# Optimization experiments

Hardware: AMD Instinct MI355X
Metric: run time of the kernel (lower is better)

The kernel has to match this reference:

```python
import jax, jax.numpy as jnp
import numpy as np

N_NODES = 50000
N_EDGES = 800000
IN_DIM = 128
OUT_DIM = 64
REL_DIM = 32
NEG_SLOPE = 0.01  # torch F.leaky_relu default


def setup_inputs() -> dict:
    key = jax.random.key(0)
    k1, k2, k3, k4, k5, k6 = jax.random.split(key, 6)
    h = jax.random.normal(k1, (N_NODES, IN_DIM), dtype=jnp.float32)
    p = jax.random.normal(k2, (N_EDGES, REL_DIM), dtype=jnp.float32)
    src = jax.random.randint(k3, (N_EDGES,), 0, N_NODES, dtype=jnp.int32)
    dst = jax.random.randint(k4, (N_EDGES,), 0, N_NODES, dtype=jnp.int32)
    # torch Linear weights: [out_features, in_features], xavier-like scale
    W_fc = jax.random.normal(k5, (OUT_DIM, IN_DIM), dtype=jnp.float32) * (2.0 / (IN_DIM + OUT_DIM)) ** 0.5
    W_attn = jax.random.normal(k6, (1, 2 * OUT_DIM + REL_DIM), dtype=jnp.float32) * 0.1
    return {"h": h, "p": p, "src": src, "dst": dst, "W_fc": W_fc, "W_attn": W_attn}


def reference(h, p, src, dst, W_fc, W_attn):
    n = h.shape[0]
    z = h @ W_fc.T                       # [N, out_dim]
    z_src = z[src]                       # [E, out_dim] gather
    z_dst = z[dst]                       # [E, out_dim] gather
    feat = jnp.concatenate([z_src, p, z_dst], axis=1)  # [E, 2*out+rel]
    a = feat @ W_attn.T                  # [E, 1]
    e = jax.nn.leaky_relu(a[:, 0], NEG_SLOPE)          # [E]
    # segment softmax over incoming edges of each dst node
    seg_max = jax.ops.segment_max(e, dst, num_segments=n)  # [N]
    num = jnp.exp(e - seg_max[dst])                        # [E]
    denom = jax.ops.segment_sum(num, dst, num_segments=n)  # [N]
    alpha = num / denom[dst]                               # [E]
    # softmax-weighted message aggregation (scatter-add)
    h_out = jax.ops.segment_sum(alpha[:, None] * z_src, dst, num_segments=n)  # [N, out_dim]
    return h_out
```

## Files before the change

kernel.cpp:

```cpp
#include <hip/hip_runtime.h>
#include <hip/hip_bf16.h>

#define N_NODES 50000
#define N_EDGES 800000
#define IN_DIM 128
#define OUT_DIM 64
#define REL_DIM 32
#define NEG_SLOPE 0.01f
#define NB 391
#define K3_TILE 2048
#define K3_BLOCKS ((N_EDGES + K3_TILE - 1) / K3_TILE)
#define BWIN 2560

typedef __attribute__((ext_vector_type(8))) short bf16x8;
typedef __attribute__((ext_vector_type(4))) float f32x4;

__device__ __forceinline__ short f2bf(float f) {
    unsigned u = __float_as_uint(f);
    u += 0x7FFF + ((u >> 16) & 1);
    return (short)(u >> 16);
}

__global__ __launch_bounds__(256) void k1_mfma(const float* __restrict__ h,
                                               const float* __restrict__ Wfc,
                                               const float* __restrict__ Wattn,
                                               __hip_bfloat16* __restrict__ zb,
                                               float* __restrict__ s1,
                                               float* __restrict__ s2,
                                               unsigned* __restrict__ ccur) {
    const int t = threadIdx.x;
    if (blockIdx.x == 0) {
        for (int i = t; i < NB * 16; i += 256) ccur[i] = 0u;
    }
    const int nt = blockIdx.x * 4 + (t >> 6);
    if (nt >= 3125) return;
    const int lane = t & 63;
    const int r = lane & 15;
    const int g = lane >> 4;
    const int n0 = nt * 16;

    const float4* hrow = (const float4*)(h + (size_t)(n0 + r) * IN_DIM);
    f32x4 acc[4] = {{0.f,0.f,0.f,0.f},{0.f,0.f,0.f,0.f},{0.f,0.f,0.f,0.f},{0.f,0.f,0.f,0.f}};

#pragma unroll
    for (int kq = 0; kq < 4; ++kq) {
        float4 h0 = hrow[kq * 8 + g * 2];
        float4 h1 = hrow[kq * 8 + g * 2 + 1];
        bf16x8 hb;
        hb[0] = f2bf(h0.x); hb[1] = f2bf(h0.y); hb[2] = f2bf(h0.z); hb[3] = f2bf(h0.w);
        hb[4] = f2bf(h1.x); hb[5] = f2bf(h1.y); hb[6] = f2bf(h1.z); hb[7] = f2bf(h1.w);
#pragma unroll
        for (int ct = 0; ct < 4; ++ct) {
            const float4* wrow = (const float4*)(Wfc + (size_t)(ct * 16 + r) * IN_DIM);
            float4 w0 = wrow[kq * 8 + g * 2];
            float4 w1 = wrow[kq * 8 + g * 2 + 1];
            bf16x8 wb;
            wb[0] = f2bf(w0.x); wb[1] = f2bf(w0.y); wb[2] = f2bf(w0.z); wb[3] = f2bf(w0.w);
            wb[4] = f2bf(w1.x); wb[5] = f2bf(w1.y); wb[6] = f2bf(w1.z); wb[7] = f2bf(w1.w);
            acc[ct] = __builtin_amdgcn_mfma_f32_16x16x32_bf16(wb, hb, acc[ct], 0, 0, 0);
        }
    }

    float r1 = 0.f, r2 = 0.f;
#pragma unroll
    for (int ct = 0; ct < 4; ++ct) {
#pragma unroll
        for (int i = 0; i < 4; ++i) {
            int c = ct * 16 + g * 4 + i;
            r1 += acc[ct][i] * Wattn[c];
            r2 += acc[ct][i] * Wattn[96 + c];
        }
        ushort4 st;
        st.x = (ushort)f2bf(acc[ct][0]); st.y = (ushort)f2bf(acc[ct][1]);
        st.z = (ushort)f2bf(acc[ct][2]); st.w = (ushort)f2bf(acc[ct][3]);
        ((ushort4*)zb)[(size_t)(n0 + r) * 16 + ct * 4 + g] = st;
    }
    r1 += __shfl_xor(r1, 16, 64); r1 += __shfl_xor(r1, 32, 64);
    r2 += __shfl_xor(r2, 16, 64); r2 += __shfl_xor(r2, 32, 64);
    if (g == 0) { s1[n0 + r] = r1; s2[n0 + r] = r2; }
}

__global__ __launch_bounds__(256) void k2_dotp(const float* __restrict__ p,
                                               const float* __restrict__ Wattn,
                                               float* __restrict__ dotp) {
    const int t = threadIdx.x;
    const int lane = t & 63;
    const int wv = blockIdx.x * 4 + (t >> 6);
    const int q = lane & 7;
    const float w0 = Wattn[64 + q * 4 + 0];
    const float w1 = Wattn[64 + q * 4 + 1];
    const float w2 = Wattn[64 + q * 4 + 2];
    const float w3 = Wattn[64 + q * 4 + 3];
    const float4* p4 = (const float4*)p;
#pragma unroll
    for (int c = 0; c < 2; ++c) {
        const int grp = wv * 2 + c;
        if (grp < 12500) {
            const int base4 = grp * 512;
            float4 v[8];
#pragma unroll
            for (int j = 0; j < 8; ++j) v[j] = p4[base4 + j * 64 + lane];
            float d[8];
#pragma unroll
            for (int j = 0; j < 8; ++j)
                d[j] = v[j].x * w0 + v[j].y * w1 + v[j].z * w2 + v[j].w * w3;
#pragma unroll
            for (int off = 1; off < 8; off <<= 1)
#pragma unroll
                for (int j = 0; j < 8; ++j) d[j] += __shfl_xor(d[j], off, 64);
            float val = 0.f;
#pragma unroll
            for (int j = 0; j < 8; ++j) {
                float tmp = __shfl(d[j], (lane & 7) * 8, 64);
                if ((lane >> 3) == j) val = tmp;
            }
            dotp[grp * 64 + lane] = val;
        }
    }
}

__global__ __launch_bounds__(256) void k3_fused(const float* __restrict__ dotp,
                                                const int* __restrict__ src,
                                                const int* __restrict__ dst,
                                                const float* __restrict__ s1,
                                                const float* __restrict__ s2,
                                                unsigned* __restrict__ ccur,
                                                float2* __restrict__ pair) {
    __shared__ unsigned hist[NB];
    __shared__ unsigned gb[NB];
    __shared__ unsigned lcur[NB];
    const int t = threadIdx.x;
    for (int i = t; i < NB; i += 256) hist[i] = 0;
    __syncthreads();

    const int base = blockIdx.x * K3_TILE;
    float evr[8];
    unsigned auxr[8];
    short br[8];
#pragma unroll
    for (int i = 0; i < 8; ++i) {
        int e = base + i * 256 + t;
        if (e < N_EDGES) {
            int s = src[e], d = dst[e];
            float a = s1[s] + dotp[e] + s2[d];
            evr[i] = a > 0.f ? a : NEG_SLOPE * a;
            auxr[i] = (unsigned)s | ((unsigned)(d & 127) << 16);
            int bb = d >> 7;
            br[i] = (short)bb;
            atomicAdd(&hist[bb], 1u);
        } else br[i] = -1;
    }
    __syncthreads();
    for (int i = t; i < NB; i += 256) {
        lcur[i] = 0;
        gb[i] = hist[i] ? (i * BWIN + atomicAdd(&ccur[i * 16], hist[i])) : 0u;
    }
    __syncthreads();
#pragma unroll
    for (int i = 0; i < 8; ++i) {
        if (br[i] >= 0) {
            int bb = br[i];
            unsigned pos = atomicAdd(&lcur[bb], 1u);
            pair[gb[bb] + pos] = make_float2(evr[i], __uint_as_float(auxr[i]));
        }
    }
}

__global__ __launch_bounds__(256) void k3b_sort(const unsigned* __restrict__ ccur,
                                                const float2* __restrict__ pair,
                                                float2* __restrict__ pair2,
                                                unsigned* __restrict__ beg_g,
                                                unsigned* __restrict__ end_g) {
    __shared__ float2 items[BWIN];
    __shared__ unsigned hist[128], loffs[128], lcur[128], sd[128];
    const int t = threadIdx.x;
    const int b = blockIdx.x;
    const int base = b * BWIN;
    int cnt = (int)ccur[b * 16];
    if (cnt > BWIN) cnt = BWIN;
    if (t < 128) { hist[t] = 0; lcur[t] = 0; }
    __syncthreads();
    for (int i = t; i < cnt; i += 256) {
        float2 it = pair[base + i];
        items[i] = it;
        atomicAdd(&hist[__float_as_uint(it.y) >> 16], 1u);
    }
    __syncthreads();
    unsigned v = (t < 128) ? hist[t] : 0u;
    if (t < 128) sd[t] = v;
    __syncthreads();
#pragma unroll
    for (int off = 1; off < 128; off <<= 1) {
        unsigned tmp = (t >= off && t < 128) ? sd[t - off] : 0u;
        __syncthreads();
        if (t < 128) sd[t] += tmp;
        __syncthreads();
    }
    if (t < 128) {
        unsigned ex = sd[t] - v;
        loffs[t] = ex;
        beg_g[b * 128 + t] = base + ex;
        end_g[b * 128 + t] = base + ex + v;
    }
    __syncthreads();
    for (int i = t; i < cnt; i += 256) {
        float2 it = items[i];
        unsigned dl = __float_as_uint(it.y) >> 16;
        unsigned pos = atomicAdd(&lcur[dl], 1u);
        pair2[base + loffs[dl] + pos] = it;
    }
}

__global__ __launch_bounds__(256) void k4_agg(const unsigned* __restrict__ beg_g,
                                              const unsigned* __restrict__ end_g,
                                              const float2* __restrict__ pair2,
                                              const __hip_bfloat16* __restrict__ zb,
                                              float* __restrict__ out) {
    const int t = threadIdx.x;
    const int lane = t & 63;
    const int sub = lane >> 4;
    const int lc = lane & 15;
    const int wid = (blockIdx.x * 256 + t) >> 6;
    const int n = wid * 4 + sub;
    const int lo = beg_g[n], hi = end_g[n];
    const ushort* zs = (const ushort*)zb;
    float a0 = 0.f, a1 = 0.f, a2 = 0.f, a3 = 0.f, den = 0.f;
    int i = lo;
    for (; i + 3 < hi; i += 4) {
        float2 pr[4];
#pragma unroll
        for (int j = 0; j < 4; ++j) pr[j] = pair2[i + j];
        ushort4 zv[4];
#pragma unroll
        for (int j = 0; j < 4; ++j) {
            int s = __float_as_uint(pr[j].y) & 0xFFFF;
            zv[j] = *(const ushort4*)&zs[s * OUT_DIM + lc * 4];
        }
#pragma unroll
        for (int j = 0; j < 4; ++j) {
            float e = __expf(pr[j].x);
            a0 += e * __uint_as_float((unsigned)zv[j].x << 16);
            a1 += e * __uint_as_float((unsigned)zv[j].y << 16);
            a2 += e * __uint_as_float((unsigned)zv[j].z << 16);
            a3 += e * __uint_as_float((unsigned)zv[j].w << 16);
            den += e;
        }
    }
    for (; i < hi; ++i) {
        float2 p0 = pair2[i];
        int s = __float_as_uint(p0.y) & 0xFFFF;
        ushort4 zv = *(const ushort4*)&zs[s * OUT_DIM + lc * 4];
        float e = __expf(p0.x);
        a0 += e * __uint_as_float((unsigned)zv.x << 16);
        a1 += e * __uint_as_float((unsigned)zv.y << 16);
        a2 += e * __uint_as_float((unsigned)zv.z << 16);
        a3 += e * __uint_as_float((unsigned)zv.w << 16);
        den += e;
    }
    float4 st;
    if (hi > lo) {
        float inv = 1.f / den;
        st.x = a0 * inv; st.y = a1 * inv; st.z = a2 * inv; st.w = a3 * inv;
    } else {
        st.x = st.y = st.z = st.w = 0.f;
    }
    ((float4*)out)[(size_t)n * 16 + lc] = st;
}

extern "C" void kernel_launch(void* const* d_in, const int* in_sizes, int n_in,
                              void* d_out, int out_size, void* d_ws, size_t ws_size,
                              hipStream_t stream) {
    const float* h     = (const float*)d_in[0];
    const float* p     = (const float*)d_in[1];
    const int*   src   = (const int*)d_in[2];
    const int*   dst   = (const int*)d_in[3];
    const float* Wfc   = (const float*)d_in[4];
    const float* Wattn = (const float*)d_in[5];
    float* out = (float*)d_out;

    float* ws = (float*)d_ws;
    __hip_bfloat16* zb = (__hip_bfloat16*)ws;
    float*    s1     = ws + 1600000;
    float*    s2     = ws + 1650000;
    float*    dotp   = ws + 1700000;
    unsigned* ccur   = (unsigned*)(ws + 2500000);
    unsigned* beg_g  = (unsigned*)(ws + 2506272);
    unsigned* end_g  = (unsigned*)(ws + 2556320);
    float2*   pair   = (float2*)(ws + 2606368);
    float2*   pair2  = (float2*)(ws + 4608288);

    k1_mfma<<<782, 256, 0, stream>>>(h, Wfc, Wattn, zb, s1, s2, ccur);
    k2_dotp<<<1564, 256, 0, stream>>>(p, Wattn, dotp);
    k3_fused<<<K3_BLOCKS, 256, 0, stream>>>(dotp, src, dst, s1, s2, ccur, pair);
    k3b_sort<<<NB, 256, 0, stream>>>(ccur, pair, pair2, beg_g, end_g);
    k4_agg<<<3125, 256, 0, stream>>>(beg_g, end_g, pair2, zb, out);
}
```

Baseline: 93.50 us.

## Fuse node projection and edge relation dot-product into one kernel launch

Merges the MFMA node-projection kernel and the p·W_attn edge dot-product kernel into one launch of 25000 blocks. The first 782 blocks also do the projection, and every block reduces one float4 per thread with three shuffles instead of the old eight-row-per-wave batched scheme. This removes a launch and lets the projection overlap the streaming of p, at the cost of many more small blocks and only one load in flight per thread. The ccur zeroing moves from block 0 to block 782.

```diff
diff --git a/kernel.cpp b/kernel.cpp
--- a/kernel.cpp
+++ b/kernel.cpp
@@ -11,6 +11,7 @@
 #define K3_TILE 2048
 #define K3_BLOCKS ((N_EDGES + K3_TILE - 1) / K3_TILE)
 #define BWIN 2560
+#define K12_GRID 25000
 
 typedef __attribute__((ext_vector_type(8))) short bf16x8;
 typedef __attribute__((ext_vector_type(4))) float f32x4;
@@ -21,101 +22,86 @@
     return (short)(u >> 16);
 }
 
-__global__ __launch_bounds__(256) void k1_mfma(const float* __restrict__ h,
-                                               const float* __restrict__ Wfc,
-                                               const float* __restrict__ Wattn,
-                                               __hip_bfloat16* __restrict__ zb,
-                                               float* __restrict__ s1,
-                                               float* __restrict__ s2,
-                                               unsigned* __restrict__ ccur) {
-    const int t = threadIdx.x;
-    if (blockIdx.x == 0) {
+__global__ __launch_bounds__(256) void k12_fused(const float* __restrict__ h,
+                                                 const float* __restrict__ Wfc,
+                                                 const float* __restrict__ Wattn,
+                                                 const float* __restrict__ p,
+                                                 __hip_bfloat16* __restrict__ zb,
+                                                 float* __restrict__ s1,
+                                                 float* __restrict__ s2,
+                                                 float* __restrict__ dotp,
+                                                 unsigned* __restrict__ ccur) {
+    const int t = threadIdx.x;
+    const int b = blockIdx.x;
+
+    if (b == 782) {
         for (int i = t; i < NB * 16; i += 256) ccur[i] = 0u;
     }
-    const int nt = blockIdx.x * 4 + (t >> 6);
-    if (nt >= 3125) return;
-    const int lane = t & 63;
-    const int r = lane & 15;
-    const int g = lane >> 4;
-    const int n0 = nt * 16;
-
-    const float4* hrow = (const float4*)(h + (size_t)(n0 + r) * IN_DIM);
-    f32x4 acc[4] = {{0.f,0.f,0.f,0.f},{0.f,0.f,0.f,0.f},{0.f,0.f,0.f,0.f},{0.f,0.f,0.f,0.f}};
-
-#pragma unroll
-    for (int kq = 0; kq < 4; ++kq) {
-        float4 h0 = hrow[kq * 8 + g * 2];
-        float4 h1 = hrow[kq * 8 + g * 2 + 1];
-        bf16x8 hb;
-        hb[0] = f2bf(h0.x); hb[1] = f2bf(h0.y); hb[2] = f2bf(h0.z); hb[3] = f2bf(h0.w);
-        hb[4] = f2bf(h1.x); hb[5] = f2bf(h1.y); hb[6] = f2bf(h1.z); hb[7] = f2bf(h1.w);
-#pragma unroll
-        for (int ct = 0; ct < 4; ++ct) {
-            const float4* wrow = (const float4*)(Wfc + (size_t)(ct * 16 + r) * IN_DIM);
-            float4 w0 = wrow[kq * 8 + g * 2];
-            float4 w1 = wrow[kq * 8 + g * 2 + 1];
-            bf16x8 wb;
-            wb[0] = f2bf(w0.x); wb[1] = f2bf(w0.y); wb[2] = f2bf(w0.z); wb[3] = f2bf(w0.w);
-            wb[4] = f2bf(w1.x); wb[5] = f2bf(w1.y); wb[6] = f2bf(w1.z); wb[7] = f2bf(w1.w);
-            acc[ct] = __builtin_amdgcn_mfma_f32_16x16x32_bf16(wb, hb, acc[ct], 0, 0, 0);
-        }
-    }
-
-    float r1 = 0.f, r2 = 0.f;
-#pragma unroll
-    for (int ct = 0; ct < 4; ++ct) {
-#pragma unroll
-        for (int i = 0; i < 4; ++i) {
-            int c = ct * 16 + g * 4 + i;
-            r1 += acc[ct][i] * Wattn[c];
-            r2 += acc[ct][i] * Wattn[96 + c];
-        }
-        ushort4 st;
-        st.x = (ushort)f2bf(acc[ct][0]); st.y = (ushort)f2bf(acc[ct][1]);
-        st.z = (ushort)f2bf(acc[ct][2]); st.w = (ushort)f2bf(acc[ct][3]);
-        ((ushort4*)zb)[(size_t)(n0 + r) * 16 + ct * 4 + g] = st;
-    }
-    r1 += __shfl_xor(r1, 16, 64); r1 += __shfl_xor(r1, 32, 64);
-    r2 += __shfl_xor(r2, 16, 64); r2 += __shfl_xor(r2, 32, 64);
-    if (g == 0) { s1[n0 + r] = r1; s2[n0 + r] = r2; }
-}
-
-__global__ __launch_bounds__(256) void k2_dotp(const float* __restrict__ p,
-                                               const float* __restrict__ Wattn,
-                                               float* __restrict__ dotp) {
-    const int t = threadIdx.x;
-    const int lane = t & 63;
-    const int wv = blockIdx.x * 4 + (t >> 6);
-    const int q = lane & 7;
-    const float w0 = Wattn[64 + q * 4 + 0];
-    const float w1 = Wattn[64 + q * 4 + 1];
-    const float w2 = Wattn[64 + q * 4 + 2];
-    const float w3 = Wattn[64 + q * 4 + 3];
-    const float4* p4 = (const float4*)p;
-#pragma unroll
-    for (int c = 0; c < 2; ++c) {
-        const int grp = wv * 2 + c;
-        if (grp < 12500) {
-            const int base4 = grp * 512;
-            float4 v[8];
-#pragma unroll
-            for (int j = 0; j < 8; ++j) v[j] = p4[base4 + j * 64 + lane];
-            float d[8];
-#pragma unroll
-            for (int j = 0; j < 8; ++j)
-                d[j] = v[j].x * w0 + v[j].y * w1 + v[j].z * w2 + v[j].w * w3;
-#pragma unroll
-            for (int off = 1; off < 8; off <<= 1)
-#pragma unroll
-                for (int j = 0; j < 8; ++j) d[j] += __shfl_xor(d[j], off, 64);
-            float val = 0.f;
-#pragma unroll
-            for (int j = 0; j < 8; ++j) {
-                float tmp = __shfl(d[j], (lane & 7) * 8, 64);
-                if ((lane >> 3) == j) val = tmp;
+
+    if (b < 782) {
+        const int nt = b * 4 + (t >> 6);
+        if (nt < 3125) {
+            const int lane = t & 63;
+            const int r = lane & 15;
+            const int g = lane >> 4;
+            const int n0 = nt * 16;
+
+            const float4* hrow = (const float4*)(h + (size_t)(n0 + r) * IN_DIM);
+            f32x4 acc[4] = {{0.f,0.f,0.f,0.f},{0.f,0.f,0.f,0.f},
+                            {0.f,0.f,0.f,0.f},{0.f,0.f,0.f,0.f}};
+
+#pragma unroll
+            for (int kq = 0; kq < 4; ++kq) {
+                float4 h0 = hrow[kq * 8 + g * 2];
+                float4 h1 = hrow[kq * 8 + g * 2 + 1];
+                bf16x8 hb;
+                hb[0] = f2bf(h0.x); hb[1] = f2bf(h0.y); hb[2] = f2bf(h0.z); hb[3] = f2bf(h0.w);
+                hb[4] = f2bf(h1.x); hb[5] = f2bf(h1.y); hb[6] = f2bf(h1.z); hb[7] = f2bf(h1.w);
+#pragma unroll
+                for (int ct = 0; ct < 4; ++ct) {
+                    const float4* wrow = (const float4*)(Wfc + (size_t)(ct * 16 + r) * IN_DIM);
+                    float4 w0 = wrow[kq * 8 + g * 2];
+                    float4 w1 = wrow[kq * 8 + g * 2 + 1];
+                    bf16x8 wb;
+                    wb[0] = f2bf(w0.x); wb[1] = f2bf(w0.y); wb[2] = f2bf(w0.z); wb[3] = f2bf(w0.w);
+                    wb[4] = f2bf(w1.x); wb[5] = f2bf(w1.y); wb[6] = f2bf(w1.z); wb[7] = f2bf(w1.w);
+                    acc[ct] = __builtin_amdgcn_mfma_f32_16x16x32_bf16(wb, hb, acc[ct], 0, 0, 0);
+                }
             }
-            dotp[grp * 64 + lane] = val;
-        }
+
+            float r1 = 0.f, r2 = 0.f;
+#pragma unroll
+            for (int ct = 0; ct < 4; ++ct) {
+#pragma unroll
+                for (int i = 0; i < 4; ++i) {
+                    int c = ct * 16 + g * 4 + i;
+                    r1 += acc[ct][i] * Wattn[c];
+                    r2 += acc[ct][i] * Wattn[96 + c];
+                }
+                ushort4 st;
+                st.x = (ushort)f2bf(acc[ct][0]); st.y = (ushort)f2bf(acc[ct][1]);
+                st.z = (ushort)f2bf(acc[ct][2]); st.w = (ushort)f2bf(acc[ct][3]);
+                ((ushort4*)zb)[(size_t)(n0 + r) * 16 + ct * 4 + g] = st;
+            }
+            r1 += __shfl_xor(r1, 16, 64); r1 += __shfl_xor(r1, 32, 64);
+            r2 += __shfl_xor(r2, 16, 64); r2 += __shfl_xor(r2, 32, 64);
+            if (g == 0) { s1[n0 + r] = r1; s2[n0 + r] = r2; }
+        }
+    }
+
+    {
+        const int idx = b * 256 + t;
+        const int q = t & 7;
+        const float w0 = Wattn[64 + q * 4 + 0];
+        const float w1 = Wattn[64 + q * 4 + 1];
+        const float w2 = Wattn[64 + q * 4 + 2];
+        const float w3 = Wattn[64 + q * 4 + 3];
+        float4 v = ((const float4*)p)[idx];
+        float d = v.x * w0 + v.y * w1 + v.z * w2 + v.w * w3;
+        d += __shfl_xor(d, 1, 64);
+        d += __shfl_xor(d, 2, 64);
+        d += __shfl_xor(d, 4, 64);
+        if (q == 0) dotp[idx >> 3] = d;
     }
 }
 
@@ -289,8 +275,7 @@
     float2*   pair   = (float2*)(ws + 2606368);
     float2*   pair2  = (float2*)(ws + 4608288);
 
-    k1_mfma<<<782, 256, 0, stream>>>(h, Wfc, Wattn, zb, s1, s2, ccur);
-    k2_dotp<<<1564, 256, 0, stream>>>(p, Wattn, dotp);
+    k12_fused<<<K12_GRID, 256, 0, stream>>>(h, Wfc, Wattn, p, zb, s1, s2, dotp, ccur);
     k3_fused<<<K3_BLOCKS, 256, 0, stream>>>(dotp, src, dst, s1, s2, ccur, pair);
     k3b_sort<<<NB, 256, 0, stream>>>(ccur, pair, pair2, beg_g, end_g);
     k4_agg<<<3125, 256, 0, stream>>>(beg_g, end_g, pair2, zb, out);
```

Result: faster. 87.56 us (-6.4%).
